# Kernel tuning notes

Measured on AMD Instinct MI355X. Metric: run time of the kernel, lower is better.

Reference implementation:

```python
import jax, jax.numpy as jnp
import numpy as np

OUTPUT_SIZE = 7
STRIDES = (4, 8, 16, 32)


def setup_inputs() -> dict:
    key = jax.random.key(0)
    ks = jax.random.split(key, 8)
    B, N, C, IMG = 2, 512, 256, 1024
    inp = {}
    for i, s in enumerate(STRIDES):
        hw = IMG // s
        inp[f"fm{i + 2}"] = jax.random.normal(ks[i], (B, hw, hw, C), dtype=jnp.float32)
    # ROIs in pixel xyxy coords, sizes spread so all FPN levels are exercised
    w = jax.random.uniform(ks[4], (B, N), minval=32.0, maxval=600.0)
    h = jax.random.uniform(ks[5], (B, N), minval=32.0, maxval=600.0)
    x1 = jax.random.uniform(ks[6], (B, N)) * (IMG - w)
    y1 = jax.random.uniform(ks[7], (B, N)) * (IMG - h)
    inp["rois"] = jnp.stack([x1, y1, x1 + w, y1 + h], axis=-1)
    inp["valid_mask"] = jnp.ones((B, N), dtype=bool)
    inp["roi_size_pred"] = N
    return inp


def _crop_and_resize(fm, boxes, size):
    # fm: [H, W, C]; boxes: [N, 4] normalized (y1, x1, y2, x2)
    # Replicates tf.image.crop_and_resize (bilinear, extrapolation_value=0).
    H, W, _ = fm.shape
    y1, x1, y2, x2 = boxes[:, 0], boxes[:, 1], boxes[:, 2], boxes[:, 3]
    g = jnp.arange(size, dtype=jnp.float32) / (size - 1)  # [S]
    ys = (y1[:, None] + g[None, :] * (y2 - y1)[:, None]) * (H - 1)  # [N, S]
    xs = (x1[:, None] + g[None, :] * (x2 - x1)[:, None]) * (W - 1)  # [N, S]
    vy = (ys >= 0.0) & (ys <= H - 1.0)
    vx = (xs >= 0.0) & (xs <= W - 1.0)
    ysc = jnp.clip(ys, 0.0, H - 1.0)
    xsc = jnp.clip(xs, 0.0, W - 1.0)
    y0 = jnp.floor(ysc).astype(jnp.int32)
    x0 = jnp.floor(xsc).astype(jnp.int32)
    yl = ysc - y0  # lerp weights
    xl = xsc - x0
    y1i = jnp.minimum(y0 + 1, H - 1)
    x1i = jnp.minimum(x0 + 1, W - 1)
    tl = fm[y0[:, :, None], x0[:, None, :]]   # [N, S, S, C]
    tr = fm[y0[:, :, None], x1i[:, None, :]]
    bl = fm[y1i[:, :, None], x0[:, None, :]]
    br = fm[y1i[:, :, None], x1i[:, None, :]]
    top = tl + (tr - tl) * xl[:, None, :, None]
    bot = bl + (br - bl) * xl[:, None, :, None]
    out = top + (bot - top) * yl[:, :, None, None]
    mask = (vy[:, :, None] & vx[:, None, :])[..., None]
    return jnp.where(mask, out, 0.0)


def _level_feats(fm, rois, stride, size):
    # fm: [H, W, C]; rois: [N, 4] pixel xyxy
    H, W = fm.shape[0], fm.shape[1]
    b = rois / stride
    boxes = jnp.stack([b[:, 1] / H, b[:, 0] / W, b[:, 3] / H, b[:, 2] / W], axis=1)
    return _crop_and_resize(fm, boxes, size).astype(jnp.float16)


def _forward(fms, rois):
    # FPN level assignment per ROI (Mask R-CNN heuristic)
    roi_w = rois[..., 2] - rois[..., 0]
    roi_h = rois[..., 3] - rois[..., 1]
    area = roi_w * roi_h
    lv = jnp.log(jnp.sqrt(area) / 224.0) / jnp.log(2.0) + 4.0
    lv = jnp.clip(jnp.round(lv).astype(jnp.int32), 2, 5) - 2  # [B, N] in [0, 3]
    per = []
    for fm, stride in zip(fms, STRIDES):
        per.append(jax.vmap(_level_feats, in_axes=(0, 0, None, None))(fm, rois, float(stride), OUTPUT_SIZE))
    stacked = jnp.stack(per, axis=0)  # [4, B, N, S, S, C] fp16
    B, N = rois.shape[0], rois.shape[1]
    return stacked[lv, jnp.arange(B)[:, None], jnp.arange(N)[None, :]]  # [B, N, S, S, C]


def reference(fm2, fm3, fm4, fm5, rois, valid_mask, roi_size_pred):
    # valid_mask / roi_size_pred are carried through per the original signature but unused in the math
    return _forward((fm2, fm3, fm4, fm5), rois)
```

## Files before the change

### kernel.cpp

```cpp
#include <hip/hip_runtime.h>
#include <hip/hip_bf16.h>


#define B_SZ   2
#define N_ROI  512
#define CCH    256
#define OUT_S  7

__global__ __launch_bounds__(256)
void roialign_kernel(const float* __restrict__ fm2,
                     const float* __restrict__ fm3,
                     const float* __restrict__ fm4,
                     const float* __restrict__ fm5,
                     const float* __restrict__ rois,
                     float* __restrict__ out)
{
    const int bn = blockIdx.x;
    const int b  = bn >> 9;
    const int t  = threadIdx.x;

    const float4 roi = ((const float4*)rois)[bn];
    const float x1 = roi.x, y1 = roi.y;
    const float w  = roi.z - roi.x;
    const float h  = roi.w - roi.y;

    float lvf = log2f(sqrtf(w * h) * (1.0f / 224.0f)) + 4.0f;
    int lv = (int)rintf(lvf);
    lv = min(max(lv, 2), 5) - 2;

    const float* fms[4] = { fm2, fm3, fm4, fm5 };
    const int    hws[4] = { 256, 128, 64, 32 };
    const float  strd[4] = { 4.0f, 8.0f, 16.0f, 32.0f };

    const int    H      = hws[lv];
    const float  stride = strd[lv];
    const float* fm     = fms[lv] + (size_t)b * (size_t)H * (size_t)H * CCH;

    __shared__ int   s_c0[2][OUT_S];
    __shared__ int   s_c1[2][OUT_S];
    __shared__ float s_fr[2][OUT_S];
    __shared__ int   s_vd[2][OUT_S];

    if (t < 2 * OUT_S) {
        const int axis = (t < OUT_S) ? 0 : 1;
        const int j    = (axis == 0) ? t : t - OUT_S;
        const float lo  = (axis == 0) ? y1 : x1;
        const float ext = (axis == 0) ? h  : w;
        const float g = (float)j * (1.0f / 6.0f);
        const float coord = (lo + g * ext) * ((float)(H - 1) / (stride * (float)H));
        const int valid = (coord >= 0.0f) && (coord <= (float)(H - 1));
        float cl = fminf(fmaxf(coord, 0.0f), (float)(H - 1));
        int c0 = (int)floorf(cl);
        float fr = cl - (float)c0;
        int c1 = min(c0 + 1, H - 1);
        s_c0[axis][j] = c0;
        s_c1[axis][j] = c1;
        s_fr[axis][j] = fr;
        s_vd[axis][j] = valid;
    }
    __syncthreads();

    const int sub  = t >> 6;
    const int lane = t & 63;
    const int c    = lane * 4;

    const size_t outBase = (size_t)bn * (OUT_S * OUT_S) * CCH;

    for (int cb = 0; cb < OUT_S * OUT_S; cb += 4) {
        const int cell = cb + sub;
        if (cell >= OUT_S * OUT_S) break;
        const int jy = cell / OUT_S;
        const int ix = cell - jy * OUT_S;

        const int   y0  = s_c0[0][jy];
        const int   y1i = s_c1[0][jy];
        const float yl  = s_fr[0][jy];
        const int   x0  = s_c0[1][ix];
        const int   x1i = s_c1[1][ix];
        const float xl  = s_fr[1][ix];
        const int   vld = s_vd[0][jy] & s_vd[1][ix];

        const float* rowT = fm + (size_t)y0  * H * CCH;
        const float* rowB = fm + (size_t)y1i * H * CCH;

        const float4 tl = *(const float4*)(rowT + x0  * CCH + c);
        const float4 tr = *(const float4*)(rowT + x1i * CCH + c);
        const float4 bl = *(const float4*)(rowB + x0  * CCH + c);
        const float4 br = *(const float4*)(rowB + x1i * CCH + c);

        float4 o;
        {
            const float tx = tl.x + (tr.x - tl.x) * xl;
            const float bx = bl.x + (br.x - bl.x) * xl;
            o.x = tx + (bx - tx) * yl;
        }
        {
            const float ty = tl.y + (tr.y - tl.y) * xl;
            const float by = bl.y + (br.y - bl.y) * xl;
            o.y = ty + (by - ty) * yl;
        }
        {
            const float tz = tl.z + (tr.z - tl.z) * xl;
            const float bz = bl.z + (br.z - bl.z) * xl;
            o.z = tz + (bz - tz) * yl;
        }
        {
            const float tw = tl.w + (tr.w - tl.w) * xl;
            const float bw = bl.w + (br.w - bl.w) * xl;
            o.w = tw + (bw - tw) * yl;
        }
        if (!vld) { o.x = 0.0f; o.y = 0.0f; o.z = 0.0f; o.w = 0.0f; }

        *(float4*)(out + outBase + (size_t)cell * CCH + c) = o;
    }
}

extern "C" void kernel_launch(void* const* d_in, const int* in_sizes, int n_in,
                              void* d_out, int out_size, void* d_ws, size_t ws_size,
                              hipStream_t stream) {
    const float* fm2  = (const float*)d_in[0];
    const float* fm3  = (const float*)d_in[1];
    const float* fm4  = (const float*)d_in[2];
    const float* fm5  = (const float*)d_in[3];
    const float* rois = (const float*)d_in[4];
    float* out = (float*)d_out;

    dim3 grid(B_SZ * N_ROI);
    dim3 block(256);
    hipLaunchKernelGGL(roialign_kernel, grid, block, 0, stream,
                       fm2, fm3, fm4, fm5, rois, out);
}
```

Before: 226.4 us.

## Map one wavefront per output cell and use nontemporal stores

The launch changes from one block per ROI looping over 49 cells to one wavefront per (ROI, cell), so the grid grows 49x/4 blocks. Each wave computes its own sample coordinates directly, which removes the shared-memory setup and the __syncthreads. Output is written with nontemporal stores to avoid polluting cache. In exchange, the ROI load and level computation are repeated per cell, and the larger grid must hide gather latency through more parallelism rather than per-thread loop work.

```diff
diff --git a/kernel.cpp b/kernel.cpp
--- a/kernel.cpp
+++ b/kernel.cpp
@@ -1,11 +1,13 @@
 #include <hip/hip_runtime.h>
-#include <hip/hip_bf16.h>
 
 
 #define B_SZ   2
 #define N_ROI  512
 #define CCH    256
 #define OUT_S  7
+#define NCELL  (OUT_S * OUT_S)
+
+typedef float nfloat4 __attribute__((ext_vector_type(4)));
 
 __global__ __launch_bounds__(256)
 void roialign_kernel(const float* __restrict__ fm2,
@@ -15,9 +17,12 @@
                      const float* __restrict__ rois,
                      float* __restrict__ out)
 {
-    const int bn = blockIdx.x;
-    const int b  = bn >> 9;
-    const int t  = threadIdx.x;
+    const int wid  = (blockIdx.x << 2) + (threadIdx.x >> 6);
+    const int bn   = wid / NCELL;
+    const int cell = wid - bn * NCELL;
+    const int b    = bn >> 9;
+    const int jy   = cell / OUT_S;
+    const int ix   = cell - jy * OUT_S;
 
     const float4 roi = ((const float4*)rois)[bn];
     const float x1 = roi.x, y1 = roi.y;
@@ -28,91 +33,64 @@
     int lv = (int)rintf(lvf);
     lv = min(max(lv, 2), 5) - 2;
 
-    const float* fms[4] = { fm2, fm3, fm4, fm5 };
-    const int    hws[4] = { 256, 128, 64, 32 };
-    const float  strd[4] = { 4.0f, 8.0f, 16.0f, 32.0f };
+    const float* fm = (lv == 0) ? fm2 : (lv == 1) ? fm3 : (lv == 2) ? fm4 : fm5;
+    const int    H      = 256 >> lv;
+    const float  stride = (float)(4 << lv);
+    const float  scale  = (float)(H - 1) / (stride * (float)H);
 
-    const int    H      = hws[lv];
-    const float  stride = strd[lv];
-    const float* fm     = fms[lv] + (size_t)b * (size_t)H * (size_t)H * CCH;
+    const float gy = (float)jy * (1.0f / 6.0f);
+    const float gx = (float)ix * (1.0f / 6.0f);
+    const float cy = (y1 + gy * h) * scale;
+    const float cx = (x1 + gx * w) * scale;
 
-    __shared__ int   s_c0[2][OUT_S];
-    __shared__ int   s_c1[2][OUT_S];
-    __shared__ float s_fr[2][OUT_S];
-    __shared__ int   s_vd[2][OUT_S];
+    const int vld = (cy >= 0.0f) & (cy <= (float)(H - 1)) &
+                    (cx >= 0.0f) & (cx <= (float)(H - 1));
 
-    if (t < 2 * OUT_S) {
-        const int axis = (t < OUT_S) ? 0 : 1;
-        const int j    = (axis == 0) ? t : t - OUT_S;
-        const float lo  = (axis == 0) ? y1 : x1;
-        const float ext = (axis == 0) ? h  : w;
-        const float g = (float)j * (1.0f / 6.0f);
-        const float coord = (lo + g * ext) * ((float)(H - 1) / (stride * (float)H));
-        const int valid = (coord >= 0.0f) && (coord <= (float)(H - 1));
-        float cl = fminf(fmaxf(coord, 0.0f), (float)(H - 1));
-        int c0 = (int)floorf(cl);
-        float fr = cl - (float)c0;
-        int c1 = min(c0 + 1, H - 1);
-        s_c0[axis][j] = c0;
-        s_c1[axis][j] = c1;
-        s_fr[axis][j] = fr;
-        s_vd[axis][j] = valid;
+    const float cyc = fminf(fmaxf(cy, 0.0f), (float)(H - 1));
+    const float cxc = fminf(fmaxf(cx, 0.0f), (float)(H - 1));
+    const int   y0  = (int)floorf(cyc);
+    const int   x0  = (int)floorf(cxc);
+    const float yl  = cyc - (float)y0;
+    const float xl  = cxc - (float)x0;
+    const int   y1i = min(y0 + 1, H - 1);
+    const int   x1i = min(x0 + 1, H - 1);
+
+    const int c = (threadIdx.x & 63) * 4;
+
+    const float* base = fm + (size_t)b * (size_t)H * (size_t)H * CCH;
+    const float* rowT = base + (size_t)y0  * H * CCH;
+    const float* rowB = base + (size_t)y1i * H * CCH;
+
+    const float4 tl = *(const float4*)(rowT + x0  * CCH + c);
+    const float4 tr = *(const float4*)(rowT + x1i * CCH + c);
+    const float4 bl = *(const float4*)(rowB + x0  * CCH + c);
+    const float4 br = *(const float4*)(rowB + x1i * CCH + c);
+
+    nfloat4 o;
+    {
+        const float tx = tl.x + (tr.x - tl.x) * xl;
+        const float bx = bl.x + (br.x - bl.x) * xl;
+        o.x = tx + (bx - tx) * yl;
     }
-    __syncthreads();
+    {
+        const float ty = tl.y + (tr.y - tl.y) * xl;
+        const float by = bl.y + (br.y - bl.y) * xl;
+        o.y = ty + (by - ty) * yl;
+    }
+    {
+        const float tz = tl.z + (tr.z - tl.z) * xl;
+        const float bz = bl.z + (br.z - bl.z) * xl;
+        o.z = tz + (bz - tz) * yl;
+    }
+    {
+        const float tw = tl.w + (tr.w - tl.w) * xl;
+        const float bw = bl.w + (br.w - bl.w) * xl;
+        o.w = tw + (bw - tw) * yl;
+    }
+    if (!vld) { o.x = 0.0f; o.y = 0.0f; o.z = 0.0f; o.w = 0.0f; }
 
-    const int sub  = t >> 6;
-    const int lane = t & 63;
-    const int c    = lane * 4;
-
-    const size_t outBase = (size_t)bn * (OUT_S * OUT_S) * CCH;
-
-    for (int cb = 0; cb < OUT_S * OUT_S; cb += 4) {
-        const int cell = cb + sub;
-        if (cell >= OUT_S * OUT_S) break;
-        const int jy = cell / OUT_S;
-        const int ix = cell - jy * OUT_S;
-
-        const int   y0  = s_c0[0][jy];
-        const int   y1i = s_c1[0][jy];
-        const float yl  = s_fr[0][jy];
-        const int   x0  = s_c0[1][ix];
-        const int   x1i = s_c1[1][ix];
-        const float xl  = s_fr[1][ix];
-        const int   vld = s_vd[0][jy] & s_vd[1][ix];
-
-        const float* rowT = fm + (size_t)y0  * H * CCH;
-        const float* rowB = fm + (size_t)y1i * H * CCH;
-
-        const float4 tl = *(const float4*)(rowT + x0  * CCH + c);
-        const float4 tr = *(const float4*)(rowT + x1i * CCH + c);
-        const float4 bl = *(const float4*)(rowB + x0  * CCH + c);
-        const float4 br = *(const float4*)(rowB + x1i * CCH + c);
-
-        float4 o;
-        {
-            const float tx = tl.x + (tr.x - tl.x) * xl;
-            const float bx = bl.x + (br.x - bl.x) * xl;
-            o.x = tx + (bx - tx) * yl;
-        }
-        {
-            const float ty = tl.y + (tr.y - tl.y) * xl;
-            const float by = bl.y + (br.y - bl.y) * xl;
-            o.y = ty + (by - ty) * yl;
-        }
-        {
-            const float tz = tl.z + (tr.z - tl.z) * xl;
-            const float bz = bl.z + (br.z - bl.z) * xl;
-            o.z = tz + (bz - tz) * yl;
-        }
-        {
-            const float tw = tl.w + (tr.w - tl.w) * xl;
-            const float bw = bl.w + (br.w - bl.w) * xl;
-            o.w = tw + (bw - tw) * yl;
-        }
-        if (!vld) { o.x = 0.0f; o.y = 0.0f; o.z = 0.0f; o.w = 0.0f; }
-
-        *(float4*)(out + outBase + (size_t)cell * CCH + c) = o;
-    }
+    nfloat4* dst = (nfloat4*)(out + (size_t)bn * NCELL * CCH + (size_t)cell * CCH + c);
+    __builtin_nontemporal_store(o, dst);
 }
 
 extern "C" void kernel_launch(void* const* d_in, const int* in_sizes, int n_in,
@@ -125,7 +103,7 @@
     const float* rois = (const float*)d_in[4];
     float* out = (float*)d_out;
 
-    dim3 grid(B_SZ * N_ROI);
+    dim3 grid((B_SZ * N_ROI * NCELL) / 4);
     dim3 block(256);
     hipLaunchKernelGGL(roialign_kernel, grid, block, 0, stream,
                        fm2, fm3, fm4, fm5, rois, out);
```

Result: faster. 218.9 us (-3.3%).
